# Kernel optimization log

Hardware: AMD Instinct MI355X
Metric: run time of the kernel (lower is better)

Reference implementation:

```python
import jax, jax.numpy as jnp
import numpy as np

N, D, K = 131072, 512, 1024


def setup_inputs() -> dict:
    key = jax.random.key(0)
    k1, k2 = jax.random.split(key)
    features = jax.random.normal(k1, (N, D), dtype=jnp.float32)
    centroids = jax.random.normal(k2, (D, K), dtype=jnp.float32)
    return {"features": features, "centroids": centroids}


def reference(features, centroids):
    # Squared Euclidean distance via norm expansion (avoids [N, D, K] broadcast):
    x_sq = jnp.sum(features * features, axis=1, keepdims=True)      # [N, 1]
    c_sq = jnp.sum(centroids * centroids, axis=0, keepdims=True)    # [1, K]
    cross = jnp.einsum('nd,dk->nk', features, centroids)            # [N, K]
    distances = x_sq - 2.0 * cross + c_sq                           # [N, K]
    assignments = jnp.argmin(distances, axis=-1)                    # [N]
    return assignments[:, None].astype(jnp.float32)                 # [N, 1]
```

## Files before the change

### kernel.cpp

```cpp
#include <hip/hip_runtime.h>
#include <hip/hip_bf16.h>

#define NPTS 131072
#define DIMS 512
#define KC   1024

typedef _Float16 f16;
using f16x8  = __attribute__((ext_vector_type(8))) _Float16;
using f32x16 = __attribute__((ext_vector_type(16))) float;
typedef unsigned short u16;
typedef unsigned int u32;
typedef unsigned long long u64;

#define CT_OFF     0ull
#define CSQ_OFF    1048576ull
#define CSQP_OFF   1052672ull
#define CNT_OFF    1118208ull
#define LIST_OFF   1118464ull
#define WS_NEEDED  1642752ull

#define MARGIN 0.2f

__device__ __forceinline__ u32 f2o(float f) {
    u32 u = __float_as_uint(f);
    return (u & 0x80000000u) ? ~u : (u | 0x80000000u);
}
__device__ __forceinline__ float o2f(u32 o) {
    u32 u = (o & 0x80000000u) ? (o & 0x7FFFFFFFu) : ~o;
    return __uint_as_float(u);
}
__device__ __forceinline__ u64 umin64(u64 a, u64 b) { return a < b ? a : b; }
__device__ __forceinline__ u64 umax64(u64 a, u64 b) { return a > b ? a : b; }

__device__ __forceinline__ void async_load16(const void* g, const void* l) {
    auto gp = reinterpret_cast<__attribute__((address_space(1))) void*>(
        reinterpret_cast<uintptr_t>(g));
    auto lp = reinterpret_cast<__attribute__((address_space(3))) void*>(
        (unsigned int)reinterpret_cast<uintptr_t>(l));
    __builtin_amdgcn_global_load_lds(gp, lp, 16, 0, 0);
}

__global__ void split_c_kernel(const float* __restrict__ C,
                               u16* __restrict__ ct, float* __restrict__ csq_part) {
    __shared__ float t[32][33];
    int bn = blockIdx.x, bd = blockIdx.y;
    int tx = threadIdx.x & 31, ty = threadIdx.x >> 5;
#pragma unroll
    for (int r = 0; r < 32; r += 8)
        t[ty + r][tx] = C[(size_t)(bd * 32 + ty + r) * KC + bn * 32 + tx];
    __syncthreads();
#pragma unroll
    for (int r = 0; r < 32; r += 8) {
        int n = bn * 32 + ty + r, d = bd * 32 + tx;
        float v = t[tx][ty + r];
        f16 h = (f16)v;
        ct[(size_t)n * DIMS + d] = *reinterpret_cast<u16*>(&h);
        float sq = v * v;
#pragma unroll
        for (int m = 1; m < 32; m <<= 1)
            sq += __shfl_xor(sq, m, 64);
        if (tx == 0) csq_part[bd * KC + n] = sq;
    }
}

__global__ void csq_reduce_kernel(const float* __restrict__ part, float* __restrict__ csq) {
    int k = blockIdx.x * 256 + threadIdx.x;
    float s = 0.f;
#pragma unroll
    for (int p = 0; p < 16; ++p) s += part[p * KC + k];
    csq[k] = s;
}

__global__ void csq_kernel(const float* __restrict__ C, float* __restrict__ csq) {
    int k = blockIdx.x * blockDim.x + threadIdx.x;
    if (k < KC) {
        float s = 0.f;
        for (int d = 0; d < DIMS; ++d) {
            float v = C[d * KC + k];
            s = fmaf(v, v, s);
        }
        csq[k] = s;
    }
}

__global__ __launch_bounds__(512, 2) void gemm_argmin_kernel(
    const float* __restrict__ F, const u16* __restrict__ Ct,
    const float* __restrict__ csq, float* __restrict__ out,
    u32* __restrict__ cnt, u32* __restrict__ list)
{
    __shared__ __align__(16) uint8_t smem[16384];
    __shared__ float csq_l[1024];
    __shared__ u32 lcnt, lbase;
    __shared__ u32 lrows[128];

    const int tid  = threadIdx.x;
    const int lane = tid & 63;
    const int wid  = tid >> 6;
    const int wm   = wid >> 2;
    const int wn   = wid & 3;
    const int py   = (int)blockIdx.x;

    const int kh = lane >> 5;
    const int cl = lane & 31;

    for (int i = tid; i < 1024; i += 512) csq_l[i] = csq[i];
    if (tid == 0) lcnt = 0;

    const float* fRow = F + (size_t)(py * 128 + wn * 32 + cl) * DIMS + kh * 8;
    f16x8 b_reg[32];
#pragma unroll
    for (int kt = 0; kt < 16; ++kt)
#pragma unroll
        for (int s = 0; s < 2; ++s) {
            float4 x0 = *(const float4*)(fRow + kt * 32 + s * 16);
            float4 x1 = *(const float4*)(fRow + kt * 32 + s * 16 + 4);
            f16x8 h;
            h[0] = (f16)x0.x; h[1] = (f16)x0.y; h[2] = (f16)x0.z; h[3] = (f16)x0.w;
            h[4] = (f16)x1.x; h[5] = (f16)x1.y; h[6] = (f16)x1.z; h[7] = (f16)x1.w;
            b_reg[kt * 2 + s] = h;
        }

    const int lr   = lane >> 2;
    const int c_st = (lane & 3) ^ ((lane >> 3) & 3);
    const u16* aStage = Ct + (size_t)(wid * 16 + lr) * DIMS + c_st * 8;
    const unsigned awdst = (unsigned)(wid * 1024);

    const int xr = (cl >> 1) & 3;
    const unsigned mbase = (unsigned)cl * 64;
    const unsigned offs[2] = { mbase + (unsigned)(((0 + kh) ^ xr) * 16),
                               mbase + (unsigned)(((2 + kh) ^ xr) * 16) };

    u64 bestA = ~0ull, bestB = ~0ull;
    f32x16 acc[2];

    async_load16(aStage, smem + awdst);
    __syncthreads();

    for (int cx = 0; cx < 8; ++cx) {
        const size_t cxoff = (size_t)cx * (128 * DIMS);
#pragma unroll
        for (int e = 0; e < 16; ++e) { acc[0][e] = 0.f; acc[1][e] = 0.f; }

#pragma unroll
        for (int kt = 0; kt < 16; ++kt) {
            if (!(cx == 7 && kt == 15)) {
                const size_t noff = (kt == 15) ? (cxoff + (size_t)(128 * DIMS))
                                               : (cxoff + (size_t)((kt + 1) * 32));
                async_load16(aStage + noff,
                             smem + (((kt + 1) & 1) ? 8192u : 0u) + awdst);
            }
            const unsigned buf = (kt & 1) ? 8192u : 0u;
#pragma unroll
            for (int s = 0; s < 2; ++s) {
                f16x8 a0 = *(const f16x8*)(smem + buf + wm * 4096 + 0 * 2048 + offs[s]);
                f16x8 a1 = *(const f16x8*)(smem + buf + wm * 4096 + 1 * 2048 + offs[s]);
                acc[0] = __builtin_amdgcn_mfma_f32_32x32x16_f16(a0, b_reg[kt * 2 + s], acc[0], 0, 0, 0);
                acc[1] = __builtin_amdgcn_mfma_f32_32x32x16_f16(a1, b_reg[kt * 2 + s], acc[1], 0, 0, 0);
            }
            __syncthreads();
        }

#pragma unroll
        for (int mt = 0; mt < 2; ++mt)
#pragma unroll
            for (int reg = 0; reg < 16; ++reg) {
                const int rl = wm * 64 + mt * 32 + (reg & 3) + 8 * (reg >> 2) + 4 * kh;
                const float d = fmaf(-2.0f, acc[mt][reg], csq_l[cx * 128 + rl]);
                const u64 key = ((u64)f2o(d) << 32) | (u32)(cx * 128 + rl);
                const u64 t = umin64(bestA, key);
                bestB = umin64(bestB, umax64(bestA, key));
                bestA = t;
            }
    }

    {
        const u64 oa = __shfl_xor(bestA, 32, 64);
        const u64 ob = __shfl_xor(bestB, 32, 64);
        const u64 lo = umin64(bestA, oa);
        const u64 bb = umin64(umax64(bestA, oa), umin64(bestB, ob));
        u64* tbl = (u64*)smem;
        if (kh == 0) {
            const int p = wn * 32 + cl;
            tbl[(p * 2 + wm) * 2 + 0] = lo;
            tbl[(p * 2 + wm) * 2 + 1] = bb;
        }
    }
    __syncthreads();

    if (tid < 128) {
        u64* tbl = (u64*)smem;
        const u64 a0 = tbl[tid * 4 + 0], b0 = tbl[tid * 4 + 1];
        const u64 a1 = tbl[tid * 4 + 2], b1 = tbl[tid * 4 + 3];
        const u64 m1 = umin64(a0, a1);
        const u64 m2 = umin64(umax64(a0, a1), umin64(b0, b1));
        const int row = py * 128 + tid;
        const float d1 = o2f((u32)(m1 >> 32));
        const float d2 = o2f((u32)(m2 >> 32));
        if (d2 - d1 > MARGIN) {
            out[row] = (float)(u32)(m1 & 1023u);
        } else {
            u32 li = atomicAdd(&lcnt, 1u);
            lrows[li] = (u32)row;
        }
    }
    __syncthreads();
    if (tid == 0 && lcnt > 0) lbase = atomicAdd(cnt, lcnt);
    __syncthreads();
    if (tid < lcnt) list[lbase + tid] = lrows[tid];
}

__global__ __launch_bounds__(256) void rescue2_kernel(
    const float* __restrict__ F, const float* __restrict__ C,
    const float* __restrict__ csq, const u32* __restrict__ cnt,
    const u32* __restrict__ list, u32* __restrict__ wptr, float* __restrict__ out)
{
    __shared__ float xs[4][512];
    __shared__ u64 wavemin[4][4];
    __shared__ int rows_s[4];

    const int tid = threadIdx.x;
    const int lane = tid & 63;
    const int wid = tid >> 6;
    const u32 n = cnt[0];

    for (;;) {
        __syncthreads();
        u32 base;
        if (tid == 0) {
            base = atomicAdd(wptr, 4u);
            rows_s[0] = (int)base;
        }
        __syncthreads();
        base = (u32)rows_s[0];
        if (base >= n) break;

        int rows[4];
#pragma unroll
        for (int j = 0; j < 4; ++j) {
            u32 idx = base + j;
            rows[j] = (int)list[idx < n ? idx : (n - 1)];
        }
#pragma unroll
        for (int j = 0; j < 4; ++j) {
            if (tid < 128)
                *(float4*)&xs[j][tid * 4] = *(const float4*)&F[(size_t)rows[j] * DIMS + tid * 4];
        }
        __syncthreads();

        float dot[4][4];
#pragma unroll
        for (int j = 0; j < 4; ++j)
#pragma unroll
            for (int q = 0; q < 4; ++q) dot[j][q] = 0.f;

#pragma unroll 4
        for (int d = 0; d < DIMS; ++d) {
            float cv[4];
#pragma unroll
            for (int q = 0; q < 4; ++q) cv[q] = C[d * KC + tid + 256 * q];
            float xv[4];
#pragma unroll
            for (int j = 0; j < 4; ++j) xv[j] = xs[j][d];
#pragma unroll
            for (int j = 0; j < 4; ++j)
#pragma unroll
                for (int q = 0; q < 4; ++q)
                    dot[j][q] = fmaf(xv[j], cv[q], dot[j][q]);
        }

#pragma unroll
        for (int j = 0; j < 4; ++j) {
            u64 best = ~0ull;
#pragma unroll
            for (int q = 0; q < 4; ++q) {
                const int k = tid + 256 * q;
                const float dist = csq[k] - 2.0f * dot[j][q];
                best = umin64(best, ((u64)f2o(dist) << 32) | (u32)k);
            }
#pragma unroll
            for (int off = 32; off > 0; off >>= 1)
                best = umin64(best, __shfl_xor(best, off, 64));
            if (lane == 0) wavemin[j][wid] = best;
        }
        __syncthreads();
        if (tid < 4) {
            const u32 idx = base + tid;
            if (idx < n) {
                u64 b = umin64(umin64(wavemin[tid][0], wavemin[tid][1]),
                               umin64(wavemin[tid][2], wavemin[tid][3]));
                out[list[idx]] = (float)(u32)(b & 0xFFFFFFFFull);
            }
        }
    }
}

__global__ __launch_bounds__(256, 3) void assign_kernel_fp32(
    const float* __restrict__ F, const float* __restrict__ C,
    const float* __restrict__ csq, float* __restrict__ out)
{
    __shared__ float At[32][68];
    __shared__ float Bs[32 * 256];
    __shared__ u64 best_row[64];

    const int tid = threadIdx.x;
    const int tx = tid & 31;
    const int ty = tid >> 5;
    const int n0 = blockIdx.x * 64;

    if (tid < 64) best_row[tid] = ~0ull;

    u64 best[8];
#pragma unroll
    for (int r = 0; r < 8; ++r) best[r] = ~0ull;

    const int arow = tid >> 3;
    const int ac4  = tid & 7;
    const float* Atp = &At[0][ty * 8];
    const float* Bsp = &Bs[tx * 4];

    for (int kt = 0; kt < 4; ++kt) {
        float acc[8][8];
#pragma unroll
        for (int r = 0; r < 8; ++r)
#pragma unroll
            for (int j = 0; j < 8; ++j) acc[r][j] = 0.f;

        for (int dt = 0; dt < DIMS / 32; ++dt) {
            __syncthreads();
#pragma unroll
            for (int i = 0; i < 2; ++i) {
                int row = arow + 32 * i;
                float4 av = *(const float4*)&F[(long)(n0 + row) * DIMS + dt * 32 + ac4 * 4];
                At[ac4 * 4 + 0][row] = av.x;
                At[ac4 * 4 + 1][row] = av.y;
                At[ac4 * 4 + 2][row] = av.z;
                At[ac4 * 4 + 3][row] = av.w;
            }
#pragma unroll
            for (int i = 0; i < 8; ++i) {
                int idx = tid + 256 * i;
                int d  = idx >> 6;
                int c4 = idx & 63;
                float4 bv = *(const float4*)&C[(long)(dt * 32 + d) * KC + kt * 256 + c4 * 4];
                *(float4*)&Bs[d * 256 + c4 * 4] = bv;
            }
            __syncthreads();

#pragma unroll 8
            for (int dd = 0; dd < 32; ++dd) {
                float4 a0 = *(const float4*)(Atp + dd * 68);
                float4 a1 = *(const float4*)(Atp + dd * 68 + 4);
                float4 b0 = *(const float4*)(Bsp + dd * 256);
                float4 b1 = *(const float4*)(Bsp + dd * 256 + 128);
                float a[8] = {a0.x, a0.y, a0.z, a0.w, a1.x, a1.y, a1.z, a1.w};
                float bb[8] = {b0.x, b0.y, b0.z, b0.w, b1.x, b1.y, b1.z, b1.w};
#pragma unroll
                for (int r = 0; r < 8; ++r)
#pragma unroll
                    for (int j = 0; j < 8; ++j)
                        acc[r][j] = fmaf(a[r], bb[j], acc[r][j]);
            }
        }

        float4 cs0 = *(const float4*)&csq[kt * 256 + tx * 4];
        float4 cs1 = *(const float4*)&csq[kt * 256 + 128 + tx * 4];
        float cs[8] = {cs0.x, cs0.y, cs0.z, cs0.w, cs1.x, cs1.y, cs1.z, cs1.w};
#pragma unroll
        for (int j = 0; j < 8; ++j) {
            int k = kt * 256 + ((j < 4) ? (tx * 4 + j) : (128 + tx * 4 + (j - 4)));
#pragma unroll
            for (int r = 0; r < 8; ++r) {
                float val = cs[j] - 2.0f * acc[r][j];
                u64 key = ((u64)f2o(val) << 32) | (u64)(unsigned)k;
                if (key < best[r]) best[r] = key;
            }
        }
    }

#pragma unroll
    for (int r = 0; r < 8; ++r)
        atomicMin(&best_row[ty * 8 + r], best[r]);
    __syncthreads();

    if (tid < 64)
        out[n0 + tid] = (float)(unsigned)(best_row[tid] & 0xFFFFFFFFull);
}

extern "C" void kernel_launch(void* const* d_in, const int* in_sizes, int n_in,
                              void* d_out, int out_size, void* d_ws, size_t ws_size,
                              hipStream_t stream) {
    const float* F = (const float*)d_in[0];
    const float* C = (const float*)d_in[1];
    float* out = (float*)d_out;
    char* ws = (char*)d_ws;

    if (ws_size < WS_NEEDED) {
        float* csq = (float*)d_ws;
        csq_kernel<<<KC / 256, 256, 0, stream>>>(C, csq);
        assign_kernel_fp32<<<NPTS / 64, 256, 0, stream>>>(F, C, csq, out);
        return;
    }

    u16* Ct = (u16*)(ws + CT_OFF);
    float* csq  = (float*)(ws + CSQ_OFF);
    float* csqp = (float*)(ws + CSQP_OFF);
    u32* cnt  = (u32*)(ws + CNT_OFF);
    u32* list = (u32*)(ws + LIST_OFF);

    hipMemsetAsync(cnt, 0, 8, stream);
    split_c_kernel<<<dim3(KC / 32, DIMS / 32), 256, 0, stream>>>(C, Ct, csqp);
    csq_reduce_kernel<<<KC / 256, 256, 0, stream>>>(csqp, csq);
    gemm_argmin_kernel<<<NPTS / 128, 512, 0, stream>>>(F, Ct, csq, out, cnt, list);
    rescue2_kernel<<<1024, 256, 0, stream>>>(F, C, csq, cnt, list, cnt + 1, out);
}
```

Measured before the change: 691.2 us.

## Stage half-chunk centroid tiles in large dynamic LDS to cut barriers

Replaces the 16 KB per-k-tile double buffer with 128 KB of dynamic shared memory, split into two halves that each hold eight k-tiles (half of a 128-centroid chunk). Loads for the next half are issued while the current half is consumed, which cuts block-wide barriers from one per k-tile to one per half-chunk. The first centroid tile loads are now issued before the feature rows are read and converted, so the two overlap. The cost is LDS use of about 136 KB per block, which allows only one block per CU instead of the two that launch_bounds asks for. It also keeps more asynchronous loads in flight at once.

```diff
diff --git a/kernel.cpp b/kernel.cpp
--- a/kernel.cpp
+++ b/kernel.cpp
@@ -88,7 +88,7 @@
     const float* __restrict__ csq, float* __restrict__ out,
     u32* __restrict__ cnt, u32* __restrict__ list)
 {
-    __shared__ __align__(16) uint8_t smem[16384];
+    extern __shared__ __align__(16) uint8_t dsm[];
     __shared__ float csq_l[1024];
     __shared__ u32 lcnt, lbase;
     __shared__ u32 lrows[128];
@@ -106,25 +106,29 @@
     for (int i = tid; i < 1024; i += 512) csq_l[i] = csq[i];
     if (tid == 0) lcnt = 0;
 
-    const float* fRow = F + (size_t)(py * 128 + wn * 32 + cl) * DIMS + kh * 8;
-    f16x8 b_reg[32];
-#pragma unroll
-    for (int kt = 0; kt < 16; ++kt)
-#pragma unroll
-        for (int s = 0; s < 2; ++s) {
-            float4 x0 = *(const float4*)(fRow + kt * 32 + s * 16);
-            float4 x1 = *(const float4*)(fRow + kt * 32 + s * 16 + 4);
-            f16x8 h;
-            h[0] = (f16)x0.x; h[1] = (f16)x0.y; h[2] = (f16)x0.z; h[3] = (f16)x0.w;
-            h[4] = (f16)x1.x; h[5] = (f16)x1.y; h[6] = (f16)x1.z; h[7] = (f16)x1.w;
-            b_reg[kt * 2 + s] = h;
-        }
-
     const int lr   = lane >> 2;
     const int c_st = (lane & 3) ^ ((lane >> 3) & 3);
     const u16* aStage = Ct + (size_t)(wid * 16 + lr) * DIMS + c_st * 8;
     const unsigned awdst = (unsigned)(wid * 1024);
 
+#pragma unroll
+    for (int k = 0; k < 8; ++k)
+        async_load16(aStage + k * 32, dsm + k * 8192 + awdst);
+
+    const float* fRow = F + (size_t)(py * 128 + wn * 32 + cl) * DIMS + kh * 8;
+    f16x8 b_reg[32];
+#pragma unroll
+    for (int kt = 0; kt < 16; ++kt)
+#pragma unroll
+        for (int s = 0; s < 2; ++s) {
+            float4 x0 = *(const float4*)(fRow + kt * 32 + s * 16);
+            float4 x1 = *(const float4*)(fRow + kt * 32 + s * 16 + 4);
+            f16x8 hv;
+            hv[0] = (f16)x0.x; hv[1] = (f16)x0.y; hv[2] = (f16)x0.z; hv[3] = (f16)x0.w;
+            hv[4] = (f16)x1.x; hv[5] = (f16)x1.y; hv[6] = (f16)x1.z; hv[7] = (f16)x1.w;
+            b_reg[kt * 2 + s] = hv;
+        }
+
     const int xr = (cl >> 1) & 3;
     const unsigned mbase = (unsigned)cl * 64;
     const unsigned offs[2] = { mbase + (unsigned)(((0 + kh) ^ xr) * 16),
@@ -133,44 +137,50 @@
     u64 bestA = ~0ull, bestB = ~0ull;
     f32x16 acc[2];
 
-    async_load16(aStage, smem + awdst);
-    __syncthreads();
-
-    for (int cx = 0; cx < 8; ++cx) {
-        const size_t cxoff = (size_t)cx * (128 * DIMS);
-#pragma unroll
-        for (int e = 0; e < 16; ++e) { acc[0][e] = 0.f; acc[1][e] = 0.f; }
-
-#pragma unroll
-        for (int kt = 0; kt < 16; ++kt) {
-            if (!(cx == 7 && kt == 15)) {
-                const size_t noff = (kt == 15) ? (cxoff + (size_t)(128 * DIMS))
-                                               : (cxoff + (size_t)((kt + 1) * 32));
-                async_load16(aStage + noff,
-                             smem + (((kt + 1) & 1) ? 8192u : 0u) + awdst);
-            }
-            const unsigned buf = (kt & 1) ? 8192u : 0u;
-#pragma unroll
-            for (int s = 0; s < 2; ++s) {
-                f16x8 a0 = *(const f16x8*)(smem + buf + wm * 4096 + 0 * 2048 + offs[s]);
-                f16x8 a1 = *(const f16x8*)(smem + buf + wm * 4096 + 1 * 2048 + offs[s]);
-                acc[0] = __builtin_amdgcn_mfma_f32_32x32x16_f16(a0, b_reg[kt * 2 + s], acc[0], 0, 0, 0);
-                acc[1] = __builtin_amdgcn_mfma_f32_32x32x16_f16(a1, b_reg[kt * 2 + s], acc[1], 0, 0, 0);
+    __syncthreads();
+
+    for (int c = 0; c < 8; ++c) {
+#pragma unroll
+        for (int h = 0; h < 2; ++h) {
+            if (!(c == 7 && h == 1)) {
+                const size_t nbase = (h == 0) ? ((size_t)c * 65536 + 256)
+                                              : ((size_t)(c + 1) * 65536);
+#pragma unroll
+                for (int k = 0; k < 8; ++k)
+                    async_load16(aStage + nbase + k * 32,
+                                 dsm + (h ^ 1) * 65536 + k * 8192 + awdst);
+            }
+            if (h == 0) {
+#pragma unroll
+                for (int e = 0; e < 16; ++e) { acc[0][e] = 0.f; acc[1][e] = 0.f; }
+            }
+#pragma unroll
+            for (int k = 0; k < 8; ++k) {
+#pragma unroll
+                for (int s = 0; s < 2; ++s) {
+                    const uint8_t* tile = dsm + h * 65536 + k * 8192;
+                    f16x8 a0 = *(const f16x8*)(tile + wm * 4096 + 0 * 2048 + offs[s]);
+                    f16x8 a1 = *(const f16x8*)(tile + wm * 4096 + 1 * 2048 + offs[s]);
+                    const f16x8 bv = b_reg[(h * 8 + k) * 2 + s];
+                    acc[0] = __builtin_amdgcn_mfma_f32_32x32x16_f16(a0, bv, acc[0], 0, 0, 0);
+                    acc[1] = __builtin_amdgcn_mfma_f32_32x32x16_f16(a1, bv, acc[1], 0, 0, 0);
+                }
+            }
+            if (h == 1) {
+#pragma unroll
+                for (int mt = 0; mt < 2; ++mt)
+#pragma unroll
+                    for (int reg = 0; reg < 16; ++reg) {
+                        const int rl = wm * 64 + mt * 32 + (reg & 3) + 8 * (reg >> 2) + 4 * kh;
+                        const float d = fmaf(-2.0f, acc[mt][reg], csq_l[c * 128 + rl]);
+                        const u64 key = ((u64)f2o(d) << 32) | (u32)(c * 128 + rl);
+                        const u64 t = umin64(bestA, key);
+                        bestB = umin64(bestB, umax64(bestA, key));
+                        bestA = t;
+                    }
             }
             __syncthreads();
         }
-
-#pragma unroll
-        for (int mt = 0; mt < 2; ++mt)
-#pragma unroll
-            for (int reg = 0; reg < 16; ++reg) {
-                const int rl = wm * 64 + mt * 32 + (reg & 3) + 8 * (reg >> 2) + 4 * kh;
-                const float d = fmaf(-2.0f, acc[mt][reg], csq_l[cx * 128 + rl]);
-                const u64 key = ((u64)f2o(d) << 32) | (u32)(cx * 128 + rl);
-                const u64 t = umin64(bestA, key);
-                bestB = umin64(bestB, umax64(bestA, key));
-                bestA = t;
-            }
     }
 
     {
@@ -178,7 +188,7 @@
         const u64 ob = __shfl_xor(bestB, 32, 64);
         const u64 lo = umin64(bestA, oa);
         const u64 bb = umin64(umax64(bestA, oa), umin64(bestB, ob));
-        u64* tbl = (u64*)smem;
+        u64* tbl = (u64*)dsm;
         if (kh == 0) {
             const int p = wn * 32 + cl;
             tbl[(p * 2 + wm) * 2 + 0] = lo;
@@ -188,7 +198,7 @@
     __syncthreads();
 
     if (tid < 128) {
-        u64* tbl = (u64*)smem;
+        u64* tbl = (u64*)dsm;
         const u64 a0 = tbl[tid * 4 + 0], b0 = tbl[tid * 4 + 1];
         const u64 a1 = tbl[tid * 4 + 2], b1 = tbl[tid * 4 + 3];
         const u64 m1 = umin64(a0, a1);
@@ -410,6 +420,6 @@
     hipMemsetAsync(cnt, 0, 8, stream);
     split_c_kernel<<<dim3(KC / 32, DIMS / 32), 256, 0, stream>>>(C, Ct, csqp);
     csq_reduce_kernel<<<KC / 256, 256, 0, stream>>>(csqp, csq);
-    gemm_argmin_kernel<<<NPTS / 128, 512, 0, stream>>>(F, Ct, csq, out, cnt, list);
+    gemm_argmin_kernel<<<NPTS / 128, 512, 131072, stream>>>(F, Ct, csq, out, cnt, list);
     rescue2_kernel<<<1024, 256, 0, stream>>>(F, C, csq, cnt, list, cnt + 1, out);
 }
```

Measured after the change: 684.0 us. About the same (-1.1%).
